# Kernel optimization log

Hardware: AMD Instinct MI355X
Metric: run time of the kernel (lower is better)

The kernel has to match this reference:

```python
import jax, jax.numpy as jnp
import numpy as np

NEG_SLOPE = 0.2  # PyG GATConv default negative_slope


def _gat_layer(x, src, dst, W, a_src, a_dst, b, heads, ch, concat, num_nodes):
    # x: [Nt, Fin]; W: [Fin, heads*ch]; a_src/a_dst: [heads, ch]
    xw = (x @ W).reshape(num_nodes, heads, ch)            # [Nt, H, C]
    alpha_s = jnp.sum(xw * a_src, axis=-1)                # [Nt, H]
    alpha_d = jnp.sum(xw * a_dst, axis=-1)                # [Nt, H]
    e = jax.nn.leaky_relu(alpha_s[src] + alpha_d[dst], NEG_SLOPE)  # [E, H]
    # segment softmax over destination nodes (every node has a self-loop)
    m = jax.lax.stop_gradient(jax.ops.segment_max(e, dst, num_segments=num_nodes))
    ex = jnp.exp(e - m[dst])
    denom = jax.ops.segment_sum(ex, dst, num_segments=num_nodes)
    alpha = ex / (denom[dst] + 1e-16)                     # [E, H]
    out = jax.ops.segment_sum(alpha[:, :, None] * xw[src], dst, num_segments=num_nodes)  # [Nt, H, C]
    out = out.reshape(num_nodes, heads * ch) if concat else out.mean(axis=1)
    return out + b


def setup_inputs() -> dict:
    key = jax.random.key(0)
    ks = jax.random.split(key, 12)
    B, N, IN, HID, H, OUT, E = 2, 10000, 256, 256, 2, 256, 160000
    x = jax.random.normal(ks[0], (B, N, IN), dtype=jnp.float32)
    edge_index = jax.random.randint(ks[1], (2, E), 0, N, dtype=jnp.int32)
    s_in = 1.0 / np.sqrt(IN)
    s_h = 1.0 / np.sqrt(HID)
    s_hh = 1.0 / np.sqrt(HID * H)
    W1 = jax.random.normal(ks[2], (IN, H * HID), dtype=jnp.float32) * s_in
    att_src1 = jax.random.normal(ks[3], (H, HID), dtype=jnp.float32) * s_h
    att_dst1 = jax.random.normal(ks[4], (H, HID), dtype=jnp.float32) * s_h
    b1 = jax.random.normal(ks[5], (H * HID,), dtype=jnp.float32) * 0.01
    W2 = jax.random.normal(ks[6], (H * HID, OUT), dtype=jnp.float32) * s_hh
    att_src2 = jax.random.normal(ks[7], (1, OUT), dtype=jnp.float32) * s_h
    att_dst2 = jax.random.normal(ks[8], (1, OUT), dtype=jnp.float32) * s_h
    b2 = jax.random.normal(ks[9], (OUT,), dtype=jnp.float32) * 0.01
    return {"x": x, "edge_index": edge_index, "W1": W1, "att_src1": att_src1,
            "att_dst1": att_dst1, "b1": b1, "W2": W2, "att_src2": att_src2,
            "att_dst2": att_dst2, "b2": b2}


def reference(x, edge_index, W1, att_src1, att_dst1, b1, W2, att_src2, att_dst2, b2):
    B, N, C = x.shape
    H, HID = att_src1.shape
    OUT = W2.shape[1]
    Nt = B * N
    xf = x.reshape(Nt, C)
    # batch edge index with per-graph node offsets (shared edges across batch)
    offs = (jnp.arange(B, dtype=edge_index.dtype) * N)       # [B]
    ei = (edge_index[:, None, :] + offs[None, :, None]).reshape(2, -1)  # [2, B*E]
    # add self loops (PyG GATConv default)
    loops = jnp.arange(Nt, dtype=edge_index.dtype)
    src = jnp.concatenate([ei[0], loops])
    dst = jnp.concatenate([ei[1], loops])
    h = _gat_layer(xf, src, dst, W1, att_src1, att_dst1, b1, H, HID, True, Nt)
    h = jax.nn.gelu(h, approximate=False)  # torch F.gelu default = exact erf
    out = _gat_layer(h, src, dst, W2, att_src2, att_dst2, b2, 1, OUT, False, Nt)
    return out.reshape(B, N, OUT)
```

## Files before the change

### kernel.cpp

```cpp
#include <hip/hip_runtime.h>
#include <math.h>

constexpr int B_   = 2;
constexpr int N_   = 10000;
constexpr int IN_  = 256;
constexpr int HID_ = 256;
constexpr int H1_  = 2;
constexpr int OUT_ = 256;
constexpr int E_   = 160000;
constexpr int NT_  = B_ * N_;
constexpr float SLOPE = 0.2f;
constexpr int DMAX = 128;
constexpr int MT_  = (NT_ + 63) / 64;

typedef unsigned short u16;
typedef __attribute__((ext_vector_type(8))) short short8;
typedef __attribute__((ext_vector_type(4))) float f32x4;

__device__ __forceinline__ u16 f2bf(float f) {
    unsigned int u = __float_as_uint(f);
    u += 0x7fffu + ((u >> 16) & 1u);
    return (u16)(u >> 16);
}
__device__ __forceinline__ void bf8(uint4 r, float4& lo, float4& hi) {
    lo = make_float4(__uint_as_float((r.x & 0xffffu) << 16),
                     __uint_as_float(r.x & 0xffff0000u),
                     __uint_as_float((r.y & 0xffffu) << 16),
                     __uint_as_float(r.y & 0xffff0000u));
    hi = make_float4(__uint_as_float((r.z & 0xffffu) << 16),
                     __uint_as_float(r.z & 0xffff0000u),
                     __uint_as_float((r.w & 0xffffu) << 16),
                     __uint_as_float(r.w & 0xffff0000u));
}
__device__ __forceinline__ void fma4(float4& a, float s, float4 v) {
    a.x = fmaf(s, v.x, a.x); a.y = fmaf(s, v.y, a.y);
    a.z = fmaf(s, v.z, a.z); a.w = fmaf(s, v.w, a.w);
}
__device__ __forceinline__ float lrelu(float e) { return (e < 0.f) ? SLOPE * e : e; }

__device__ __forceinline__ void g2l16(const void* g, void* l) {
    __builtin_amdgcn_global_load_lds(
        (const __attribute__((address_space(1))) unsigned int*)g,
        (__attribute__((address_space(3))) unsigned int*)l, 16, 0, 0);
}

__global__ __launch_bounds__(256) void k_wprep(
    const float* __restrict__ W1,
    const float* __restrict__ aS1, const float* __restrict__ aD1,
    const float* __restrict__ W2,
    const float* __restrict__ aS2, const float* __restrict__ aD2,
    float* __restrict__ w1s, float* __restrict__ w1d,
    float* __restrict__ w2s, float* __restrict__ w2d,
    u16* __restrict__ W1t, u16* __restrict__ W2t,
    uint4* __restrict__ zbase) {
    __shared__ float tld[32][33];
    const int blk = blockIdx.x;
    if (blk < 16) {
        for (int i = blk * 256 + threadIdx.x; i < 12500; i += 16 * 256)
            zbase[i] = make_uint4(0, 0, 0, 0);
    } else if (blk < 528) {
        int wv = (blk - 16) * 4 + (threadIdx.x >> 6);
        int lane = threadIdx.x & 63;
        int c = lane * 4;
        float4 wr, av;
        if (wv < 1024) {
            int h = (wv >> 8) & 1;
            int k = wv & 255;
            const float* a = (wv < 512) ? aS1 : aD1;
            wr = *(const float4*)(W1 + (size_t)k * 512 + h * 256 + c);
            av = *(const float4*)(a + h * 256 + c);
        } else {
            int k = (wv - 1024) & 511;
            const float* a = (wv < 1536) ? aS2 : aD2;
            wr = *(const float4*)(W2 + (size_t)k * 256 + c);
            av = *(const float4*)(a + c);
        }
        float s = wr.x * av.x + wr.y * av.y + wr.z * av.z + wr.w * av.w;
        #pragma unroll
        for (int off = 32; off; off >>= 1) s += __shfl_down(s, off);
        if (lane == 0) {
            if (wv < 512)       w1s[wv] = s;
            else if (wv < 1024) w1d[wv - 512] = s;
            else if (wv < 1536) w2s[wv - 1024] = s;
            else                w2d[wv - 1536] = s;
        }
    } else {
        const int b = blk - 528;
        const int z = b >> 7;
        const int bb = b & 127;
        const float* S = z ? W2 : W1;
        u16* D = z ? W2t : W1t;
        const int R = z ? 512 : 256;
        const int C = z ? 256 : 512;
        const int xt = C >> 5;
        const int bx = bb % xt, by = bb / xt;
        const int tx = threadIdx.x & 31, ty = threadIdx.x >> 5;
        int xx = bx * 32 + tx;
        int y0 = by * 32 + ty;
        #pragma unroll
        for (int i = 0; i < 32; i += 8)
            tld[ty + i][tx] = S[(size_t)(y0 + i) * C + xx];
        __syncthreads();
        int xo = by * 32 + tx;
        int yo = bx * 32 + ty;
        #pragma unroll
        for (int i = 0; i < 32; i += 8)
            D[(size_t)(yo + i) * R + xo] = f2bf(tld[tx][ty + i]);
    }
}

__global__ __launch_bounds__(256) void k_pre(
    const float* __restrict__ x, u16* __restrict__ Xb,
    const float* __restrict__ w1s, const float* __restrict__ w1d,
    float* __restrict__ as1, float* __restrict__ ad1,
    const int* __restrict__ ei, int* __restrict__ cnt, int* __restrict__ bucket) {
    const int NB = NT_ / 4;
    if ((int)blockIdx.x < NB) {
        const int w = threadIdx.x >> 6, lane = threadIdx.x & 63;
        const int nt = blockIdx.x * 4 + w;
        const int c = lane * 4;
        float4 v = *(const float4*)(x + (size_t)nt * 256 + c);
        ((uint2*)(Xb + (size_t)nt * 256))[lane] =
            make_uint2((unsigned)f2bf(v.x) | ((unsigned)f2bf(v.y) << 16),
                       (unsigned)f2bf(v.z) | ((unsigned)f2bf(v.w) << 16));
        float4 s0v = *(const float4*)(w1s + c);
        float4 s1v = *(const float4*)(w1s + 256 + c);
        float4 d0v = *(const float4*)(w1d + c);
        float4 d1v = *(const float4*)(w1d + 256 + c);
        float s0 = v.x*s0v.x + v.y*s0v.y + v.z*s0v.z + v.w*s0v.w;
        float s1 = v.x*s1v.x + v.y*s1v.y + v.z*s1v.z + v.w*s1v.w;
        float d0 = v.x*d0v.x + v.y*d0v.y + v.z*d0v.z + v.w*d0v.w;
        float d1 = v.x*d1v.x + v.y*d1v.y + v.z*d1v.z + v.w*d1v.w;
        #pragma unroll
        for (int off = 32; off; off >>= 1) {
            s0 += __shfl_down(s0, off); s1 += __shfl_down(s1, off);
            d0 += __shfl_down(d0, off); d1 += __shfl_down(d1, off);
        }
        if (lane == 0) {
            as1[nt * 2] = s0; as1[nt * 2 + 1] = s1;
            ad1[nt * 2] = d0; ad1[nt * 2 + 1] = d1;
        }
    } else {
        int e = (blockIdx.x - NB) * 256 + threadIdx.x;
        if (e < E_) {
            int s = ei[e], d = ei[E_ + e];
            int p = atomicAdd(&cnt[d], 1);
            if (p < DMAX - 1) bucket[d * DMAX + p] = s;
        }
    }
}

__global__ __launch_bounds__(256) void k_agg1x(
    const u16* __restrict__ Xb,
    const float* __restrict__ as_, const float* __restrict__ ad_,
    const int* __restrict__ cnt, const int* __restrict__ bucket,
    u16* __restrict__ Y) {
    __shared__ int   stl[4][DMAX];
    __shared__ float exw[4][2 * DMAX];
    const int w    = threadIdx.x >> 6;
    const int lane = threadIdx.x & 63;
    const int half = lane >> 5;
    const int l32  = lane & 31;
    const int nt   = blockIdx.x * 4 + w;
    if (nt >= NT_) return;
    const int nl   = nt % N_;
    const int boff = nt - nl;
    const int r0   = nl * DMAX;
    int deg = cnt[nl]; deg = (deg < DMAX - 1) ? deg : (DMAX - 1);
    const float adv0 = ad_[nt * 2], adv1 = ad_[nt * 2 + 1];
    const float adv = half ? adv1 : adv0;

    for (int i = lane; i <= deg; i += 64)
        stl[w][i] = (i < deg) ? (bucket[r0 + i] + boff) : nt;

    float den = 0.f;
    for (int i = l32; i <= deg; i += 32) {
        int st = stl[w][i];
        float ex = __expf(lrelu(as_[st * 2 + half] + adv));
        exw[w][2 * i + half] = ex;
        den += ex;
    }
    #pragma unroll
    for (int off = 16; off; off >>= 1) den += __shfl_xor(den, off);
    const float inv = 1.f / (den + 1e-16f);
    const float invO = __shfl_xor(inv, 32);

    const int slot = half;
    const int nin = deg + 1;
    const u16* fb = Xb + l32 * 8;
    float4 A0l = {0,0,0,0}, A0h = {0,0,0,0}, A1l = {0,0,0,0}, A1h = {0,0,0,0};
    float4 B0l = {0,0,0,0}, B0h = {0,0,0,0}, B1l = {0,0,0,0}, B1h = {0,0,0,0};
    int j = 0;
    for (; j + 8 <= nin; j += 8) {
        int sA = stl[w][j + slot],     sB = stl[w][j + 2 + slot];
        int sC = stl[w][j + 4 + slot], sD = stl[w][j + 6 + slot];
        float2 wA = *(const float2*)&exw[w][2 * (j + slot)];
        float2 wB = *(const float2*)&exw[w][2 * (j + 2 + slot)];
        float2 wC = *(const float2*)&exw[w][2 * (j + 4 + slot)];
        float2 wD = *(const float2*)&exw[w][2 * (j + 6 + slot)];
        uint4 vA = *(const uint4*)(fb + (size_t)sA * 256);
        uint4 vB = *(const uint4*)(fb + (size_t)sB * 256);
        uint4 vC = *(const uint4*)(fb + (size_t)sC * 256);
        uint4 vD = *(const uint4*)(fb + (size_t)sD * 256);
        float4 lo, hi;
        bf8(vA, lo, hi); fma4(A0l, wA.x, lo); fma4(A0h, wA.x, hi);
                         fma4(A1l, wA.y, lo); fma4(A1h, wA.y, hi);
        bf8(vB, lo, hi); fma4(B0l, wB.x, lo); fma4(B0h, wB.x, hi);
                         fma4(B1l, wB.y, lo); fma4(B1h, wB.y, hi);
        bf8(vC, lo, hi); fma4(A0l, wC.x, lo); fma4(A0h, wC.x, hi);
                         fma4(A1l, wC.y, lo); fma4(A1h, wC.y, hi);
        bf8(vD, lo, hi); fma4(B0l, wD.x, lo); fma4(B0h, wD.x, hi);
                         fma4(B1l, wD.y, lo); fma4(B1h, wD.y, hi);
    }
    for (int jj = j + slot; jj < nin; jj += 2) {
        int s0 = stl[w][jj];
        float2 w01 = *(const float2*)&exw[w][2 * jj];
        uint4 v0 = *(const uint4*)(fb + (size_t)s0 * 256);
        float4 lo, hi;
        bf8(v0, lo, hi); fma4(A0l, w01.x, lo); fma4(A0h, w01.x, hi);
                         fma4(A1l, w01.y, lo); fma4(A1h, w01.y, hi);
    }
    A0l.x += B0l.x; A0l.y += B0l.y; A0l.z += B0l.z; A0l.w += B0l.w;
    A0h.x += B0h.x; A0h.y += B0h.y; A0h.z += B0h.z; A0h.w += B0h.w;
    A1l.x += B1l.x; A1l.y += B1l.y; A1l.z += B1l.z; A1l.w += B1l.w;
    A1h.x += B1h.x; A1h.y += B1h.y; A1h.z += B1h.z; A1h.w += B1h.w;
    A0l.x += __shfl_xor(A0l.x, 32); A0l.y += __shfl_xor(A0l.y, 32);
    A0l.z += __shfl_xor(A0l.z, 32); A0l.w += __shfl_xor(A0l.w, 32);
    A0h.x += __shfl_xor(A0h.x, 32); A0h.y += __shfl_xor(A0h.y, 32);
    A0h.z += __shfl_xor(A0h.z, 32); A0h.w += __shfl_xor(A0h.w, 32);
    A1l.x += __shfl_xor(A1l.x, 32); A1l.y += __shfl_xor(A1l.y, 32);
    A1l.z += __shfl_xor(A1l.z, 32); A1l.w += __shfl_xor(A1l.w, 32);
    A1h.x += __shfl_xor(A1h.x, 32); A1h.y += __shfl_xor(A1h.y, 32);
    A1h.z += __shfl_xor(A1h.z, 32); A1h.w += __shfl_xor(A1h.w, 32);

    if (slot == 0) {
        float f0[8] = { A0l.x*inv,  A0l.y*inv,  A0l.z*inv,  A0l.w*inv,
                        A0h.x*inv,  A0h.y*inv,  A0h.z*inv,  A0h.w*inv };
        float f1[8] = { A1l.x*invO, A1l.y*invO, A1l.z*invO, A1l.w*invO,
                        A1h.x*invO, A1h.y*invO, A1h.z*invO, A1h.w*invO };
        size_t ob = (size_t)nt * 512 + l32 * 8;
        *(uint4*)(Y + ob) =
            make_uint4((unsigned)f2bf(f0[0]) | ((unsigned)f2bf(f0[1]) << 16),
                       (unsigned)f2bf(f0[2]) | ((unsigned)f2bf(f0[3]) << 16),
                       (unsigned)f2bf(f0[4]) | ((unsigned)f2bf(f0[5]) << 16),
                       (unsigned)f2bf(f0[6]) | ((unsigned)f2bf(f0[7]) << 16));
        *(uint4*)(Y + ob + 256) =
            make_uint4((unsigned)f2bf(f1[0]) | ((unsigned)f2bf(f1[1]) << 16),
                       (unsigned)f2bf(f1[2]) | ((unsigned)f2bf(f1[3]) << 16),
                       (unsigned)f2bf(f1[4]) | ((unsigned)f2bf(f1[5]) << 16),
                       (unsigned)f2bf(f1[6]) | ((unsigned)f2bf(f1[7]) << 16));
    }
}

__global__ __launch_bounds__(256, 3) void gemm_g(
    const u16* __restrict__ Yf, const u16* __restrict__ W1t,
    u16* __restrict__ Hb,
    const float* __restrict__ b1,
    const float* __restrict__ w2s, const float* __restrict__ w2d,
    float* __restrict__ as2, float* __restrict__ ad2, int M) {
    __shared__ u16 sB[64 * 256];
    __shared__ u16 sA[2][64 * 64];
    const int tid = threadIdx.x, wave = tid >> 6, lane = tid & 63;
    const int bm = blockIdx.x, bn = blockIdx.y, h = blockIdx.z;
    const int wm = wave & 1, wn = wave >> 1;
    const int l15 = lane & 15, quad = lane >> 4;

    {
        const int rl = lane >> 5;
        const int u  = lane & 31;
        #pragma unroll
        for (int i = 0; i < 8; i++) {
            int r  = wave * 16 + i * 2 + rl;
            int us = (u & ~7) | ((u & 7) ^ (r & 7));
            g2l16(W1t + (size_t)(h * 256 + bn * 64 + r) * 256 + us * 8,
                  &sB[(wave * 16 + i * 2) * 256]);
        }
    }

    const int arl = lane >> 3;
    const int au  = lane & 7;
    const int aus = au ^ arl;
    auto stageA = [&](int tm, int kb, int b) {
        #pragma unroll
        for (int i = 0; i < 2; i++) {
            int R0 = wave * 16 + i * 8;
            int rg = tm * 64 + R0 + arl;
            rg = (rg < M) ? rg : (M - 1);
            g2l16(Yf + (size_t)rg * 512 + h * 256 + kb * 64 + aus * 8,
                  &sA[b][R0 * 64]);
        }
    };

    const int rA0 = wm * 32 + l15, rA1 = rA0 + 16;
    const int rB0 = wn * 32 + l15, rB1 = rB0 + 16;

    f32x4 acc[2][2];
    #pragma unroll
    for (int i = 0; i < 2; i++)
        #pragma unroll
        for (int j = 0; j < 2; j++)
            acc[i][j] = (f32x4){0.f, 0.f, 0.f, 0.f};

    const int colL = bn * 64 + wn * 32;
    float Bv[2], Sv[2], Dv[2];
    #pragma unroll
    for (int j = 0; j < 2; j++) {
        int cg = h * 256 + colL + j * 16 + l15;
        Bv[j] = b1[cg]; Sv[j] = w2s[cg]; Dv[j] = w2d[cg];
    }

    stageA(bm, 0, 0);
    __syncthreads();
    int buf = 0;
    for (int t = bm; t < MT_; t += 64) {
        #pragma unroll
        for (int kb = 0; kb < 4; kb++) {
            int nkb = (kb + 1) & 3;
            int ntl = (kb == 3) ? t + 64 : t;
            if (ntl < MT_) stageA(ntl, nkb, buf ^ 1);
            #pragma unroll
            for (int ks = 0; ks < 2; ks++) {
                int ua = ks * 4 + quad;
                short8 a0 = *(const short8*)(&sA[buf][rA0 * 64 + (ua ^ (rA0 & 7)) * 8]);
                short8 a1 = *(const short8*)(&sA[buf][rA1 * 64 + (ua ^ (rA1 & 7)) * 8]);
                int vb = kb * 8 + ks * 4 + quad;
                short8 b0 = *(const short8*)(&sB[rB0 * 256 + ((vb & ~7) | ((vb & 7) ^ (rB0 & 7))) * 8]);
                short8 b1v = *(const short8*)(&sB[rB1 * 256 + ((vb & ~7) | ((vb & 7) ^ (rB1 & 7))) * 8]);
                acc[0][0] = __builtin_amdgcn_mfma_f32_16x16x32_bf16(a0, b0, acc[0][0], 0, 0, 0);
                acc[0][1] = __builtin_amdgcn_mfma_f32_16x16x32_bf16(a0, b1v, acc[0][1], 0, 0, 0);
                acc[1][0] = __builtin_amdgcn_mfma_f32_16x16x32_bf16(a1, b0, acc[1][0], 0, 0, 0);
                acc[1][1] = __builtin_amdgcn_mfma_f32_16x16x32_bf16(a1, b1v, acc[1][1], 0, 0, 0);
            }
            if (kb == 3) {
                #pragma unroll
                for (int i = 0; i < 2; i++) {
                    #pragma unroll
                    for (int r = 0; r < 4; r++) {
                        int row = t * 64 + wm * 32 + i * 16 + quad * 4 + r;
                        float o[2], ps = 0.f, pd = 0.f;
                        #pragma unroll
                        for (int j = 0; j < 2; j++) {
                            float v = acc[i][j][r] + Bv[j];
                            v = 0.5f * v * (1.f + erff(v * 0.70710678118654752f));
                            o[j] = v;
                            ps = fmaf(v, Sv[j], ps);
                            pd = fmaf(v, Dv[j], pd);
                        }
                        #pragma unroll
                        for (int off = 1; off < 16; off <<= 1) {
                            ps += __shfl_xor(ps, off);
                            pd += __shfl_xor(pd, off);
                        }
                        if (row < M) {
                            if (l15 == 0) { atomicAdd(&as2[row], ps); atomicAdd(&ad2[row], pd); }
                            #pragma unroll
                            for (int j = 0; j < 2; j++)
                                Hb[(size_t)row * 512 + h * 256 + colL + j * 16 + l15] = f2bf(o[j]);
                        }
                    }
                }
                #pragma unroll
                for (int i = 0; i < 2; i++)
                    #pragma unroll
                    for (int j = 0; j < 2; j++)
                        acc[i][j] = (f32x4){0.f, 0.f, 0.f, 0.f};
            }
            __syncthreads();
            buf ^= 1;
        }
    }
}

__global__ __launch_bounds__(256, 2) void gemm_p(
    const u16* __restrict__ A, const u16* __restrict__ Bt,
    u16* __restrict__ C16, int M) {
    __shared__ u16 sB[64 * 512];
    __shared__ u16 sA[2][64 * 64];
    const int tid = threadIdx.x, wave = tid >> 6, lane = tid & 63;
    const int bm = blockIdx.x, bn = blockIdx.y;
    const int wm = wave & 1, wn = wave >> 1;
    const int l15 = lane & 15, quad = lane >> 4;

    {
        const int u = lane;
        #pragma unroll
        for (int i = 0; i < 16; i++) {
            int r  = wave * 16 + i;
            int us = (u & ~7) | ((u & 7) ^ (r & 7));
            g2l16(Bt + (size_t)(bn * 64 + r) * 512 + us * 8,
                  &sB[r * 512]);
        }
    }

    const int arl = lane >> 3;
    const int au  = lane & 7;
    const int aus = au ^ arl;
    auto stageA = [&](int tm, int kb, int b) {
        #pragma unroll
        for (int i = 0; i < 2; i++) {
            int R0 = wave * 16 + i * 8;
            int rg = tm * 64 + R0 + arl;
            rg = (rg < M) ? rg : (M - 1);
            g2l16(A + (size_t)rg * 512 + kb * 64 + aus * 8,
                  &sA[b][R0 * 64]);
        }
    };

    const int rA0 = wm * 32 + l15, rA1 = rA0 + 16;
    const int rB0 = wn * 32 + l15, rB1 = rB0 + 16;

    f32x4 acc[2][2];
    #pragma unroll
    for (int i = 0; i < 2; i++)
        #pragma unroll
        for (int j = 0; j < 2; j++)
            acc[i][j] = (f32x4){0.f, 0.f, 0.f, 0.f};

    stageA(bm, 0, 0);
    __syncthreads();
    int buf = 0;
    for (int t = bm; t < MT_; t += 128) {
        #pragma unroll
        for (int kb = 0; kb < 8; kb++) {
            int nkb = (kb + 1) & 7;
            int ntl = (kb == 7) ? t + 128 : t;
            if (ntl < MT_) stageA(ntl, nkb, buf ^ 1);
            #pragma unroll
            for (int ks = 0; ks < 2; ks++) {
                int ua = ks * 4 + quad;
                short8 a0 = *(const short8*)(&sA[buf][rA0 * 64 + (ua ^ (rA0 & 7)) * 8]);
                short8 a1 = *(const short8*)(&sA[buf][rA1 * 64 + (ua ^ (rA1 & 7)) * 8]);
                int vb = kb * 8 + ks * 4 + quad;
                short8 b0 = *(const short8*)(&sB[rB0 * 512 + ((vb & ~7) | ((vb & 7) ^ (rB0 & 7))) * 8]);
                short8 b1v = *(const short8*)(&sB[rB1 * 512 + ((vb & ~7) | ((vb & 7) ^ (rB1 & 7))) * 8]);
                acc[0][0] = __builtin_amdgcn_mfma_f32_16x16x32_bf16(a0, b0, acc[0][0], 0, 0, 0);
                acc[0][1] = __builtin_amdgcn_mfma_f32_16x16x32_bf16(a0, b1v, acc[0][1], 0, 0, 0);
                acc[1][0] = __builtin_amdgcn_mfma_f32_16x16x32_bf16(a1, b0, acc[1][0], 0, 0, 0);
                acc[1][1] = __builtin_amdgcn_mfma_f32_16x16x32_bf16(a1, b1v, acc[1][1], 0, 0, 0);
            }
            if (kb == 7) {
                #pragma unroll
                for (int i = 0; i < 2; i++) {
                    #pragma unroll
                    for (int r = 0; r < 4; r++) {
                        int row = t * 64 + wm * 32 + i * 16 + quad * 4 + r;
                        if (row < M) {
                            #pragma unroll
                            for (int j = 0; j < 2; j++) {
                                int col = bn * 64 + wn * 32 + j * 16 + l15;
                                C16[(size_t)row * 256 + col] = f2bf(acc[i][j][r]);
                            }
                        }
                    }
                }
                #pragma unroll
                for (int i = 0; i < 2; i++)
                    #pragma unroll
                    for (int j = 0; j < 2; j++)
                        acc[i][j] = (f32x4){0.f, 0.f, 0.f, 0.f};
            }
            __syncthreads();
            buf ^= 1;
        }
    }
}

__global__ __launch_bounds__(256) void k_agg_h1(
    const u16* __restrict__ feat,
    const float* __restrict__ as_, const float* __restrict__ ad_,
    const int* __restrict__ cnt, const int* __restrict__ bucket,
    const float* __restrict__ bias,
    float* __restrict__ out) {
    __shared__ int   stl[4][DMAX];
    __shared__ float exw[4][DMAX];
    const int w    = threadIdx.x >> 6;
    const int lane = threadIdx.x & 63;
    const int slot = lane >> 5;
    const int l32  = lane & 31;
    const int nt   = blockIdx.x * 4 + w;
    if (nt >= NT_) return;
    const int nl   = nt % N_;
    const int boff = nt - nl;
    const int r0   = nl * DMAX;
    int deg = cnt[nl]; deg = (deg < DMAX - 1) ? deg : (DMAX - 1);
    const float adv = ad_[nt];

    for (int i = lane; i <= deg; i += 64)
        stl[w][i] = (i < deg) ? (bucket[r0 + i] + boff) : nt;

    float den = 0.f;
    for (int i = lane; i <= deg; i += 64) {
        int st = stl[w][i];
        float ex = __expf(lrelu(as_[st] + adv));
        exw[w][i] = ex;
        den += ex;
    }
    #pragma unroll
    for (int off = 32; off; off >>= 1) den += __shfl_xor(den, off);
    const float inv = 1.f / (den + 1e-16f);

    const int nin = deg + 1;
    const u16* fb = feat + l32 * 8;
    float4 aA0 = {0,0,0,0}, aB0 = {0,0,0,0}, aA1 = {0,0,0,0}, aB1 = {0,0,0,0};
    int j = 0;
    for (; j + 8 <= nin; j += 8) {
        int sA = stl[w][j + slot],     sB = stl[w][j + 2 + slot];
        int sC = stl[w][j + 4 + slot], sD = stl[w][j + 6 + slot];
        float wA = exw[w][j + slot],     wB = exw[w][j + 2 + slot];
        float wC = exw[w][j + 4 + slot], wD = exw[w][j + 6 + slot];
        uint4 vA = *(const uint4*)(fb + (size_t)sA * 256);
        uint4 vB = *(const uint4*)(fb + (size_t)sB * 256);
        uint4 vC = *(const uint4*)(fb + (size_t)sC * 256);
        uint4 vD = *(const uint4*)(fb + (size_t)sD * 256);
        float4 lo, hi;
        bf8(vA, lo, hi); fma4(aA0, wA, lo); fma4(aB0, wA, hi);
        bf8(vB, lo, hi); fma4(aA1, wB, lo); fma4(aB1, wB, hi);
        bf8(vC, lo, hi); fma4(aA0, wC, lo); fma4(aB0, wC, hi);
        bf8(vD, lo, hi); fma4(aA1, wD, lo); fma4(aB1, wD, hi);
    }
    for (; j + 4 <= nin; j += 4) {
        int sA = stl[w][j + slot], sB = stl[w][j + 2 + slot];
        float wA = exw[w][j + slot], wB = exw[w][j + 2 + slot];
        uint4 vA = *(const uint4*)(fb + (size_t)sA * 256);
        uint4 vB = *(const uint4*)(fb + (size_t)sB * 256);
        float4 lo, hi;
        bf8(vA, lo, hi); fma4(aA0, wA, lo); fma4(aB0, wA, hi);
        bf8(vB, lo, hi); fma4(aA1, wB, lo); fma4(aB1, wB, hi);
    }
    for (int jj = j + slot; jj < nin; jj += 2) {
        int s0 = stl[w][jj];
        float w0 = exw[w][jj];
        uint4 v0 = *(const uint4*)(fb + (size_t)s0 * 256);
        float4 lo, hi;
        bf8(v0, lo, hi); fma4(aA0, w0, lo); fma4(aB0, w0, hi);
    }
    aA0.x += aA1.x; aA0.y += aA1.y; aA0.z += aA1.z; aA0.w += aA1.w;
    aB0.x += aB1.x; aB0.y += aB1.y; aB0.z += aB1.z; aB0.w += aB1.w;
    aA0.x += __shfl_xor(aA0.x, 32); aA0.y += __shfl_xor(aA0.y, 32);
    aA0.z += __shfl_xor(aA0.z, 32); aA0.w += __shfl_xor(aA0.w, 32);
    aB0.x += __shfl_xor(aB0.x, 32); aB0.y += __shfl_xor(aB0.y, 32);
    aB0.z += __shfl_xor(aB0.z, 32); aB0.w += __shfl_xor(aB0.w, 32);

    if (slot == 0) {
        int c = l32 * 8;
        float4 b0 = *(const float4*)(bias + c);
        float4 b1 = *(const float4*)(bias + c + 4);
        float* ob = out + (size_t)nt * 256 + c;
        *(float4*)(ob)     = make_float4(aA0.x * inv + b0.x, aA0.y * inv + b0.y,
                                         aA0.z * inv + b0.z, aA0.w * inv + b0.w);
        *(float4*)(ob + 4) = make_float4(aB0.x * inv + b1.x, aB0.y * inv + b1.y,
                                         aB0.z * inv + b1.z, aB0.w * inv + b1.w);
    }
}

extern "C" void kernel_launch(void* const* d_in, const int* in_sizes, int n_in,
                              void* d_out, int out_size, void* d_ws, size_t ws_size,
                              hipStream_t stream) {
    const float* x    = (const float*)d_in[0];
    const int*   ei   = (const int*)  d_in[1];
    const float* W1   = (const float*)d_in[2];
    const float* aS1  = (const float*)d_in[3];
    const float* aD1  = (const float*)d_in[4];
    const float* b1   = (const float*)d_in[5];
    const float* W2   = (const float*)d_in[6];
    const float* aS2  = (const float*)d_in[7];
    const float* aD2  = (const float*)d_in[8];
    const float* b2   = (const float*)d_in[9];
    float* out = (float*)d_out;

    u16* Xb   = (u16*)d_ws;
    u16* Y    = Xb + (size_t)NT_ * 256;
    u16* Hb   = Y  + (size_t)NT_ * 512;
    u16* hw16 = Hb + (size_t)NT_ * 512;
    float* as1 = (float*)(hw16 + (size_t)NT_ * 256);
    float* ad1 = as1 + NT_ * H1_;
    float* as2 = ad1 + NT_ * H1_;
    float* ad2 = as2 + NT_;
    int* cnt   = (int*)(ad2 + NT_);
    int* bucket= cnt + N_;
    u16* W1t   = (u16*)(bucket + N_ * DMAX);
    u16* W2t   = W1t + 512 * 256;
    float* w1s = (float*)(W2t + 256 * 512);
    float* w1d = w1s + 512;
    float* w2s = w1d + 512;
    float* w2d = w2s + 512;

    k_wprep<<<784, 256, 0, stream>>>(W1, aS1, aD1, W2, aS2, aD2,
                                     w1s, w1d, w2s, w2d, W1t, W2t, (uint4*)as2);

    k_pre<<<NT_ / 4 + (E_ + 255) / 256, 256, 0, stream>>>(
        x, Xb, w1s, w1d, as1, ad1, ei, cnt, bucket);

    k_agg1x<<<(NT_ + 3) / 4, 256, 0, stream>>>(Xb, as1, ad1, cnt, bucket, Y);
    gemm_g<<<dim3(64, 4, 2), 256, 0, stream>>>(
        Y, W1t, Hb, b1, w2s, w2d, as2, ad2, NT_);

    gemm_p<<<dim3(128, 4), 256, 0, stream>>>(Hb, W2t, hw16, NT_);
    k_agg_h1<<<(NT_ + 3) / 4, 256, 0, stream>>>(hw16, as2, ad2, cnt, bucket, b2, out);
}
```

Baseline: 190.5 us.

## Swap GEMM stationarity: keep activation rows resident, stream weight tiles

Both GEMMs used to keep a weight slice resident in LDS and loop persistently over row tiles. They now give each block one row tile of activations, held in LDS, and loop over all column blocks while double-buffering the weight tiles. The grid becomes one block per row tile (313 blocks for gemm_g, 625 for gemm_p), and gemm_p drops to 32-row tiles with higher occupancy. Each activation row is now read from global memory once instead of once per column block, at the cost of re-reading the small weights from cache per block and doing less work per wave in gemm_p.

Measured after the change: 192.1 us. Within noise of the previous version (+0.8%).

```diff
diff --git a/kernel.cpp b/kernel.cpp
--- a/kernel.cpp
+++ b/kernel.cpp
@@ -11,7 +11,6 @@
 constexpr int NT_  = B_ * N_;
 constexpr float SLOPE = 0.2f;
 constexpr int DMAX = 128;
-constexpr int MT_  = (NT_ + 63) / 64;
 
 typedef unsigned short u16;
 typedef __attribute__((ext_vector_type(8))) short short8;
@@ -258,10 +257,10 @@
     const float* __restrict__ b1,
     const float* __restrict__ w2s, const float* __restrict__ w2d,
     float* __restrict__ as2, float* __restrict__ ad2, int M) {
-    __shared__ u16 sB[64 * 256];
-    __shared__ u16 sA[2][64 * 64];
+    __shared__ u16 sA[64 * 256];
+    __shared__ u16 sBd[2][64 * 64];
     const int tid = threadIdx.x, wave = tid >> 6, lane = tid & 63;
-    const int bm = blockIdx.x, bn = blockIdx.y, h = blockIdx.z;
+    const int bm = blockIdx.x, h = blockIdx.y;
     const int wm = wave & 1, wn = wave >> 1;
     const int l15 = lane & 15, quad = lane >> 4;
 
@@ -270,24 +269,24 @@
         const int u  = lane & 31;
         #pragma unroll
         for (int i = 0; i < 8; i++) {
-            int r  = wave * 16 + i * 2 + rl;
-            int us = (u & ~7) | ((u & 7) ^ (r & 7));
-            g2l16(W1t + (size_t)(h * 256 + bn * 64 + r) * 256 + us * 8,
-                  &sB[(wave * 16 + i * 2) * 256]);
-        }
-    }
-
-    const int arl = lane >> 3;
-    const int au  = lane & 7;
-    const int aus = au ^ arl;
-    auto stageA = [&](int tm, int kb, int b) {
+            int rloc = wave * 16 + i * 2 + rl;
+            int rg = bm * 64 + rloc; rg = (rg < M) ? rg : (M - 1);
+            int us = (u & ~7) | ((u & 7) ^ (rloc & 7));
+            g2l16(Yf + (size_t)rg * 512 + h * 256 + us * 8,
+                  &sA[(wave * 16 + i * 2) * 256]);
+        }
+    }
+
+    const int brl = lane >> 3;
+    const int bu  = lane & 7;
+    auto stageB = [&](int bn, int kb, int b) {
         #pragma unroll
         for (int i = 0; i < 2; i++) {
             int R0 = wave * 16 + i * 8;
-            int rg = tm * 64 + R0 + arl;
-            rg = (rg < M) ? rg : (M - 1);
-            g2l16(Yf + (size_t)rg * 512 + h * 256 + kb * 64 + aus * 8,
-                  &sA[b][R0 * 64]);
+            int r = R0 + brl;
+            int us = bu ^ (r & 7);
+            g2l16(W1t + (size_t)(h * 256 + bn * 64 + r) * 256 + kb * 64 + us * 8,
+                  &sBd[b][R0 * 64]);
         }
     };
 
@@ -301,42 +300,41 @@
         for (int j = 0; j < 2; j++)
             acc[i][j] = (f32x4){0.f, 0.f, 0.f, 0.f};
 
-    const int colL = bn * 64 + wn * 32;
-    float Bv[2], Sv[2], Dv[2];
-    #pragma unroll
-    for (int j = 0; j < 2; j++) {
-        int cg = h * 256 + colL + j * 16 + l15;
-        Bv[j] = b1[cg]; Sv[j] = w2s[cg]; Dv[j] = w2d[cg];
-    }
-
-    stageA(bm, 0, 0);
+    stageB(0, 0, 0);
     __syncthreads();
     int buf = 0;
-    for (int t = bm; t < MT_; t += 64) {
+    for (int bn = 0; bn < 4; bn++) {
         #pragma unroll
         for (int kb = 0; kb < 4; kb++) {
-            int nkb = (kb + 1) & 3;
-            int ntl = (kb == 3) ? t + 64 : t;
-            if (ntl < MT_) stageA(ntl, nkb, buf ^ 1);
+            int nbn = (kb == 3) ? bn + 1 : bn;
+            int nkb = (kb == 3) ? 0 : kb + 1;
+            if (nbn < 4) stageB(nbn, nkb, buf ^ 1);
             #pragma unroll
             for (int ks = 0; ks < 2; ks++) {
-                int ua = ks * 4 + quad;
-                short8 a0 = *(const short8*)(&sA[buf][rA0 * 64 + (ua ^ (rA0 & 7)) * 8]);
-                short8 a1 = *(const short8*)(&sA[buf][rA1 * 64 + (ua ^ (rA1 & 7)) * 8]);
-                int vb = kb * 8 + ks * 4 + quad;
-                short8 b0 = *(const short8*)(&sB[rB0 * 256 + ((vb & ~7) | ((vb & 7) ^ (rB0 & 7))) * 8]);
-                short8 b1v = *(const short8*)(&sB[rB1 * 256 + ((vb & ~7) | ((vb & 7) ^ (rB1 & 7))) * 8]);
-                acc[0][0] = __builtin_amdgcn_mfma_f32_16x16x32_bf16(a0, b0, acc[0][0], 0, 0, 0);
+                int ua = kb * 8 + ks * 4 + quad;
+                short8 a0 = *(const short8*)(&sA[rA0 * 256 + ((ua & ~7) | ((ua & 7) ^ (rA0 & 7))) * 8]);
+                short8 a1 = *(const short8*)(&sA[rA1 * 256 + ((ua & ~7) | ((ua & 7) ^ (rA1 & 7))) * 8]);
+                int ub = ks * 4 + quad;
+                short8 b0  = *(const short8*)(&sBd[buf][rB0 * 64 + (ub ^ (rB0 & 7)) * 8]);
+                short8 b1v = *(const short8*)(&sBd[buf][rB1 * 64 + (ub ^ (rB1 & 7)) * 8]);
+                acc[0][0] = __builtin_amdgcn_mfma_f32_16x16x32_bf16(a0, b0,  acc[0][0], 0, 0, 0);
                 acc[0][1] = __builtin_amdgcn_mfma_f32_16x16x32_bf16(a0, b1v, acc[0][1], 0, 0, 0);
-                acc[1][0] = __builtin_amdgcn_mfma_f32_16x16x32_bf16(a1, b0, acc[1][0], 0, 0, 0);
+                acc[1][0] = __builtin_amdgcn_mfma_f32_16x16x32_bf16(a1, b0,  acc[1][0], 0, 0, 0);
                 acc[1][1] = __builtin_amdgcn_mfma_f32_16x16x32_bf16(a1, b1v, acc[1][1], 0, 0, 0);
             }
             if (kb == 3) {
+                const int colL = bn * 64 + wn * 32;
+                float Bv[2], Sv[2], Dv[2];
+                #pragma unroll
+                for (int j = 0; j < 2; j++) {
+                    int cg = h * 256 + colL + j * 16 + l15;
+                    Bv[j] = b1[cg]; Sv[j] = w2s[cg]; Dv[j] = w2d[cg];
+                }
                 #pragma unroll
                 for (int i = 0; i < 2; i++) {
                     #pragma unroll
                     for (int r = 0; r < 4; r++) {
-                        int row = t * 64 + wm * 32 + i * 16 + quad * 4 + r;
+                        int row = bm * 64 + wm * 32 + i * 16 + quad * 4 + r;
                         float o[2], ps = 0.f, pd = 0.f;
                         #pragma unroll
                         for (int j = 0; j < 2; j++) {
@@ -371,93 +369,80 @@
     }
 }
 
-__global__ __launch_bounds__(256, 2) void gemm_p(
+__global__ __launch_bounds__(256, 3) void gemm_p(
     const u16* __restrict__ A, const u16* __restrict__ Bt,
     u16* __restrict__ C16, int M) {
-    __shared__ u16 sB[64 * 512];
-    __shared__ u16 sA[2][64 * 64];
+    __shared__ u16 sA[32 * 512];
+    __shared__ u16 sBd[2][64 * 64];
     const int tid = threadIdx.x, wave = tid >> 6, lane = tid & 63;
-    const int bm = blockIdx.x, bn = blockIdx.y;
+    const int bm = blockIdx.x;
     const int wm = wave & 1, wn = wave >> 1;
     const int l15 = lane & 15, quad = lane >> 4;
 
     {
         const int u = lane;
         #pragma unroll
-        for (int i = 0; i < 16; i++) {
-            int r  = wave * 16 + i;
-            int us = (u & ~7) | ((u & 7) ^ (r & 7));
-            g2l16(Bt + (size_t)(bn * 64 + r) * 512 + us * 8,
-                  &sB[r * 512]);
-        }
-    }
-
-    const int arl = lane >> 3;
-    const int au  = lane & 7;
-    const int aus = au ^ arl;
-    auto stageA = [&](int tm, int kb, int b) {
+        for (int i = 0; i < 8; i++) {
+            int rloc = wave * 8 + i;
+            int rg = bm * 32 + rloc; rg = (rg < M) ? rg : (M - 1);
+            int us = (u & ~7) | ((u & 7) ^ (rloc & 7));
+            g2l16(A + (size_t)rg * 512 + us * 8, &sA[rloc * 512]);
+        }
+    }
+
+    const int brl = lane >> 3;
+    const int bu  = lane & 7;
+    auto stageB = [&](int bn, int kb, int b) {
         #pragma unroll
         for (int i = 0; i < 2; i++) {
             int R0 = wave * 16 + i * 8;
-            int rg = tm * 64 + R0 + arl;
-            rg = (rg < M) ? rg : (M - 1);
-            g2l16(A + (size_t)rg * 512 + kb * 64 + aus * 8,
-                  &sA[b][R0 * 64]);
+            int r = R0 + brl;
+            int us = bu ^ (r & 7);
+            g2l16(Bt + (size_t)(bn * 64 + r) * 512 + kb * 64 + us * 8,
+                  &sBd[b][R0 * 64]);
         }
     };
 
-    const int rA0 = wm * 32 + l15, rA1 = rA0 + 16;
+    const int rA0 = wm * 16 + l15;
     const int rB0 = wn * 32 + l15, rB1 = rB0 + 16;
 
-    f32x4 acc[2][2];
-    #pragma unroll
-    for (int i = 0; i < 2; i++)
-        #pragma unroll
-        for (int j = 0; j < 2; j++)
-            acc[i][j] = (f32x4){0.f, 0.f, 0.f, 0.f};
-
-    stageA(bm, 0, 0);
+    f32x4 acc[2];
+    acc[0] = (f32x4){0.f, 0.f, 0.f, 0.f};
+    acc[1] = (f32x4){0.f, 0.f, 0.f, 0.f};
+
+    stageB(0, 0, 0);
     __syncthreads();
     int buf = 0;
-    for (int t = bm; t < MT_; t += 128) {
+    for (int bn = 0; bn < 4; bn++) {
         #pragma unroll
         for (int kb = 0; kb < 8; kb++) {
-            int nkb = (kb + 1) & 7;
-            int ntl = (kb == 7) ? t + 128 : t;
-            if (ntl < MT_) stageA(ntl, nkb, buf ^ 1);
+            int nbn = (kb == 7) ? bn + 1 : bn;
+            int nkb = (kb == 7) ? 0 : kb + 1;
+            if (nbn < 4) stageB(nbn, nkb, buf ^ 1);
             #pragma unroll
             for (int ks = 0; ks < 2; ks++) {
-                int ua = ks * 4 + quad;
-                short8 a0 = *(const short8*)(&sA[buf][rA0 * 64 + (ua ^ (rA0 & 7)) * 8]);
-                short8 a1 = *(const short8*)(&sA[buf][rA1 * 64 + (ua ^ (rA1 & 7)) * 8]);
-                int vb = kb * 8 + ks * 4 + quad;
-                short8 b0 = *(const short8*)(&sB[rB0 * 512 + ((vb & ~7) | ((vb & 7) ^ (rB0 & 7))) * 8]);
-                short8 b1v = *(const short8*)(&sB[rB1 * 512 + ((vb & ~7) | ((vb & 7) ^ (rB1 & 7))) * 8]);
-                acc[0][0] = __builtin_amdgcn_mfma_f32_16x16x32_bf16(a0, b0, acc[0][0], 0, 0, 0);
-                acc[0][1] = __builtin_amdgcn_mfma_f32_16x16x32_bf16(a0, b1v, acc[0][1], 0, 0, 0);
-                acc[1][0] = __builtin_amdgcn_mfma_f32_16x16x32_bf16(a1, b0, acc[1][0], 0, 0, 0);
-                acc[1][1] = __builtin_amdgcn_mfma_f32_16x16x32_bf16(a1, b1v, acc[1][1], 0, 0, 0);
+                int ua = kb * 8 + ks * 4 + quad;
+                short8 a0 = *(const short8*)(&sA[rA0 * 512 + ((ua & ~7) | ((ua & 7) ^ (rA0 & 7))) * 8]);
+                int ub = ks * 4 + quad;
+                short8 b0  = *(const short8*)(&sBd[buf][rB0 * 64 + (ub ^ (rB0 & 7)) * 8]);
+                short8 b1v = *(const short8*)(&sBd[buf][rB1 * 64 + (ub ^ (rB1 & 7)) * 8]);
+                acc[0] = __builtin_amdgcn_mfma_f32_16x16x32_bf16(a0, b0,  acc[0], 0, 0, 0);
+                acc[1] = __builtin_amdgcn_mfma_f32_16x16x32_bf16(a0, b1v, acc[1], 0, 0, 0);
             }
             if (kb == 7) {
                 #pragma unroll
-                for (int i = 0; i < 2; i++) {
-                    #pragma unroll
-                    for (int r = 0; r < 4; r++) {
-                        int row = t * 64 + wm * 32 + i * 16 + quad * 4 + r;
-                        if (row < M) {
-                            #pragma unroll
-                            for (int j = 0; j < 2; j++) {
-                                int col = bn * 64 + wn * 32 + j * 16 + l15;
-                                C16[(size_t)row * 256 + col] = f2bf(acc[i][j][r]);
-                            }
+                for (int r = 0; r < 4; r++) {
+                    int row = bm * 32 + wm * 16 + quad * 4 + r;
+                    if (row < M) {
+                        #pragma unroll
+                        for (int j = 0; j < 2; j++) {
+                            int col = bn * 64 + wn * 32 + j * 16 + l15;
+                            C16[(size_t)row * 256 + col] = f2bf(acc[j][r]);
                         }
                     }
                 }
-                #pragma unroll
-                for (int i = 0; i < 2; i++)
-                    #pragma unroll
-                    for (int j = 0; j < 2; j++)
-                        acc[i][j] = (f32x4){0.f, 0.f, 0.f, 0.f};
+                acc[0] = (f32x4){0.f, 0.f, 0.f, 0.f};
+                acc[1] = (f32x4){0.f, 0.f, 0.f, 0.f};
             }
             __syncthreads();
             buf ^= 1;
@@ -592,9 +577,9 @@
         x, Xb, w1s, w1d, as1, ad1, ei, cnt, bucket);
 
     k_agg1x<<<(NT_ + 3) / 4, 256, 0, stream>>>(Xb, as1, ad1, cnt, bucket, Y);
-    gemm_g<<<dim3(64, 4, 2), 256, 0, stream>>>(
+    gemm_g<<<dim3((NT_ + 63) / 64, 2), 256, 0, stream>>>(
         Y, W1t, Hb, b1, w2s, w2d, as2, ad2, NT_);
 
-    gemm_p<<<dim3(128, 4), 256, 0, stream>>>(Hb, W2t, hw16, NT_);
+    gemm_p<<<dim3((NT_ + 31) / 32), 256, 0, stream>>>(Hb, W2t, hw16, NT_);
     k_agg_h1<<<(NT_ + 3) / 4, 256, 0, stream>>>(hw16, as2, ad2, cnt, bucket, b2, out);
 }
```
